# Kernel optimization log

Measured on AMD Instinct MI355X. Metric: run time of the kernel, lower is better.

The kernel has to match this reference:

```python
import jax, jax.numpy as jnp
import numpy as np

N, E, G = 50000, 800000, 128      # nodes, edges, graphs
IN, H, OUT = 128, 128, 2          # feature dims
K, L = 3, 3                       # Chebyshev order, num conv layers
EPS = 1e-5


def setup_inputs() -> dict:
    key = jax.random.key(0)
    ks = jax.random.split(key, 10)
    x = jax.random.normal(ks[0], (N, IN), dtype=jnp.float32)
    edge_index = jax.random.randint(ks[1], (2, E), 0, N, dtype=jnp.int64)
    batch = jnp.sort(jax.random.randint(ks[2], (N,), 0, G, dtype=jnp.int64))
    w_in = jax.random.normal(ks[3], (IN, H), dtype=jnp.float32) * 0.05
    b_in = jnp.zeros((H,), jnp.float32)
    ln_g = jnp.ones((H,), jnp.float32)
    ln_b = jnp.zeros((H,), jnp.float32)
    cheb_w = jax.random.normal(ks[4], (L, K, H, H), dtype=jnp.float32) * 0.05
    cheb_b = jnp.zeros((L, H), jnp.float32)
    bn_g = jnp.ones((L, H), jnp.float32)
    bn_b = jnp.zeros((L, H), jnp.float32)
    w1 = jax.random.normal(ks[5], (H, H // 2), dtype=jnp.float32) * 0.05
    b1 = jnp.zeros((H // 2,), jnp.float32)
    w2 = jax.random.normal(ks[6], (H // 2, OUT), dtype=jnp.float32) * 0.05
    b2 = jnp.zeros((OUT,), jnp.float32)
    return dict(x=x, w_in=w_in, b_in=b_in, ln_g=ln_g, ln_b=ln_b,
                cheb_w=cheb_w, cheb_b=cheb_b, bn_g=bn_g, bn_b=bn_b,
                w1=w1, b1=b1, w2=w2, b2=b2,
                edge_index=edge_index, batch=batch)


def reference(x, w_in, b_in, ln_g, ln_b, cheb_w, cheb_b, bn_g, bn_b,
              w1, b1, w2, b2, edge_index, batch):
    src, dst = edge_index[0], edge_index[1]

    # ChebConv scaled Laplacian with lambda_max=2, sym norm:
    # L_hat = -D^{-1/2} A D^{-1/2}  (self-loop terms cancel in PyG's __norm__)
    deg = jax.ops.segment_sum(jnp.ones((E,), x.dtype), src, num_segments=N)
    dinv = jnp.where(deg > 0, jax.lax.rsqrt(jnp.maximum(deg, 1.0)), 0.0)
    w_edge = -dinv[src] * dinv[dst]  # [E]

    def spmm(h):  # y_i = sum_{(j->i)} w_edge * h_j
        return jax.ops.segment_sum(w_edge[:, None] * h[src], dst, num_segments=N)

    # node_embed: Linear -> LayerNorm -> ReLU (dropout p used in eval => identity)
    h = x @ w_in + b_in
    mu = h.mean(-1, keepdims=True)
    var = h.var(-1, keepdims=True)
    h = (h - mu) * jax.lax.rsqrt(var + EPS) * ln_g + ln_b
    h = jax.nn.relu(h)

    hiddens = [h]
    for l in range(L):
        # Chebyshev recurrence: T0 = h, T1 = L_hat h, Tk = 2 L_hat T_{k-1} - T_{k-2}
        tx0 = h
        out = tx0 @ cheb_w[l, 0]
        tx1 = spmm(tx0)
        out = out + tx1 @ cheb_w[l, 1]
        for k in range(2, K):
            tx2 = 2.0 * spmm(tx1) - tx0
            out = out + tx2 @ cheb_w[l, k]
            tx0, tx1 = tx1, tx2
        out = out + cheb_b[l]
        # BatchNorm1d over nodes (training-mode batch statistics, biased var)
        m = out.mean(0)
        v = out.var(0)
        out = (out - m) * jax.lax.rsqrt(v + EPS) * bn_g[l] + bn_b[l]
        h = jax.nn.relu(out)
        hiddens.append(h)

    # Laplacian (Dirichlet) regularization over all hidden states
    reg = jnp.float32(0.0)
    for hh in hiddens:
        diff = hh[src] - hh[dst]              # [E, H]
        reg = reg + jnp.mean(jnp.sum(diff * diff, axis=-1))
    reg = reg / len(hiddens)

    # global mean pool over batch assignment
    counts = jax.ops.segment_sum(jnp.ones((N,), x.dtype), batch, num_segments=G)
    gsum = jax.ops.segment_sum(h, batch, num_segments=G)
    gmean = gsum / jnp.maximum(counts, 1.0)[:, None]

    z = jax.nn.relu(gmean @ w1 + b1)
    logits = z @ w2 + b2
    return logits, reg
```

## Files before the change

kernel.cpp:

```cpp
#include <hip/hip_runtime.h>
#include <hip/hip_bf16.h>

#define NNODES 50000
#define NEDGES 800000
#define NGRAPH 128
#define CAP 64
#define EPSV 1e-5f

typedef __attribute__((ext_vector_type(8))) short bf16x8;
typedef __attribute__((ext_vector_type(8))) unsigned short us16x8;
typedef __attribute__((ext_vector_type(4))) float f32x4;
typedef __attribute__((ext_vector_type(2))) float f32x2;

__device__ __forceinline__ unsigned short f2bf(float f) {
    unsigned u = __float_as_uint(f);
    return (unsigned short)((u + 0x7fffu + ((u >> 16) & 1u)) >> 16);
}
__device__ __forceinline__ float bf2f(unsigned short h) {
    return __uint_as_float(((unsigned)h) << 16);
}
__device__ __forceinline__ unsigned pk4_fp8(float a, float b, float c, float d) {
    int w = __builtin_amdgcn_cvt_pk_fp8_f32(a, b, 0, false);
    w = __builtin_amdgcn_cvt_pk_fp8_f32(c, d, w, true);
    return (unsigned)w;
}

__global__ void fillA_kernel(const int* __restrict__ src, const int* __restrict__ dst,
                             int* __restrict__ outdeg, int* __restrict__ indeg,
                             unsigned* __restrict__ slot, int E) {
    int e = blockIdx.x * blockDim.x + threadIdx.x;
    if (e < E) {
        int s = src[e];
        int d = dst[e];
        atomicAdd(&outdeg[s], 1);
        int pos = atomicAdd(&indeg[d], 1);
        if (pos < CAP) slot[(size_t)d * CAP + pos] = (unsigned)s;
    }
}

__global__ void pack_kernel(unsigned* __restrict__ slot, const int* __restrict__ indeg,
                            const int* __restrict__ outdeg,
                            const int* __restrict__ batch, int* __restrict__ gstart,
                            int total, int n) {
    if (blockIdx.x == 0 && threadIdx.x <= NGRAPH) {
        int g = threadIdx.x;
        int lo = 0, hi = n;
        while (lo < hi) {
            int mid = (lo + hi) >> 1;
            if (batch[mid] < g) lo = mid + 1; else hi = mid;
        }
        gstart[g] = lo;
    }
    int i = blockIdx.x * blockDim.x + threadIdx.x;
    if (i >= total) return;
    int node = i >> 6, k = i & (CAP - 1);
    int cnt = min(indeg[node], CAP);
    if (k < cnt) {
        unsigned idx = slot[i];
        int d = outdeg[idx];
        float dv = (d > 0) ? rsqrtf((float)d) : 0.0f;
        slot[i] = idx | ((unsigned)f2bf(dv) << 16);
    }
}

__global__ void wprep_kernel(const float* __restrict__ w_in, const float* __restrict__ cheb_w,
                             unsigned short* __restrict__ Wsp) {
    int p = blockIdx.x;
    int t = threadIdx.x;
    for (int s8 = 0; s8 < 8; ++s8) {
        int slot = s8 * 256 + t;
        int kc = slot >> 9, ct = (slot >> 6) & 7, lane = slot & 63;
        int q = lane >> 4, nn = lane & 15;
        unsigned short* o = Wsp + ((size_t)p * 2048 + slot) * 16;
#pragma unroll
        for (int j = 0; j < 8; ++j) {
            int k = kc * 32 + q * 8 + j, c = ct * 16 + nn;
            float v;
            if (p == 0) {
                v = w_in[k * 128 + c];
            } else {
                int pl = (p - 1) / 3, kk = (p - 1) % 3;
                v = cheb_w[((size_t)(pl * 3 + kk) * 128 + k) * 128 + c];
                if (kk == 0) v -= cheb_w[((size_t)(pl * 3 + 2) * 128 + k) * 128 + c];
                else if (kk == 2) v *= 2.f;
            }
            unsigned short hi = f2bf(v);
            o[j] = hi;
            o[8 + j] = f2bf(v - bf2f(hi));
        }
    }
}

template <int NPARTS, int EPI, int AF32>
__global__ __launch_bounds__(256) void gemm_mfma(
    const void* __restrict__ A0v, const void* __restrict__ A1v, const void* __restrict__ A2v,
    const unsigned short* __restrict__ Wsp, const float* __restrict__ bias,
    unsigned short* __restrict__ out16,
    const float* __restrict__ g0, const float* __restrict__ b0,
    float* __restrict__ colsum, float* __restrict__ colsumsq, int n) {
    __shared__ float red[256];
    int t = threadIdx.x, w = t >> 6, l = t & 63;
    int m = l & 15, qk = l >> 4;
    int rowA = blockIdx.x * 64 + w * 16 + m;
    red[t] = 0.f;
    __syncthreads();

    f32x4 acc[8];
#pragma unroll
    for (int ct = 0; ct < 8; ++ct) acc[ct] = (f32x4){0.f, 0.f, 0.f, 0.f};

    bool valid = rowA < n;
#pragma unroll
    for (int p = 0; p < NPARTS; ++p) {
#pragma unroll
        for (int kc = 0; kc < 4; ++kc) {
            bf16x8 ah, al;
            if (AF32) {
                const float* arow = (const float*)A0v;
                if (p == 1) arow = (const float*)A1v;
                if (p == 2) arow = (const float*)A2v;
                arow += (size_t)rowA * 128;
                float4 x0, x1;
                if (valid) {
                    x0 = *(const float4*)&arow[kc * 32 + qk * 8];
                    x1 = *(const float4*)&arow[kc * 32 + qk * 8 + 4];
                } else {
                    x0 = make_float4(0.f, 0.f, 0.f, 0.f); x1 = x0;
                }
                float xs[8] = {x0.x, x0.y, x0.z, x0.w, x1.x, x1.y, x1.z, x1.w};
#pragma unroll
                for (int j = 0; j < 8; ++j) {
                    unsigned short hi = f2bf(xs[j]);
                    ah[j] = (short)hi;
                    al[j] = (short)f2bf(xs[j] - bf2f(hi));
                }
            } else {
                const unsigned short* arow = (const unsigned short*)A0v;
                if (p == 1) arow = (const unsigned short*)A1v;
                if (p == 2) arow = (const unsigned short*)A2v;
                arow += (size_t)rowA * 128;
                if (valid) ah = *(const bf16x8*)&arow[kc * 32 + qk * 8];
                else ah = (bf16x8){0, 0, 0, 0, 0, 0, 0, 0};
            }
            const unsigned short* wb = Wsp + ((size_t)((p * 4 + kc) * 8) * 64 + l) * 16;
#pragma unroll
            for (int ct = 0; ct < 8; ++ct) {
                bf16x8 bh = *(const bf16x8*)(wb + (size_t)ct * 64 * 16);
                bf16x8 bl = *(const bf16x8*)(wb + (size_t)ct * 64 * 16 + 8);
                acc[ct] = __builtin_amdgcn_mfma_f32_16x16x32_bf16(ah, bh, acc[ct], 0, 0, 0);
                if (AF32)
                    acc[ct] = __builtin_amdgcn_mfma_f32_16x16x32_bf16(al, bh, acc[ct], 0, 0, 0);
                acc[ct] = __builtin_amdgcn_mfma_f32_16x16x32_bf16(ah, bl, acc[ct], 0, 0, 0);
            }
        }
    }

    int rowC0 = blockIdx.x * 64 + w * 16 + qk * 4;
    if (EPI == 0) {
        float rs[4] = {0.f, 0.f, 0.f, 0.f}, rss[4] = {0.f, 0.f, 0.f, 0.f};
#pragma unroll
        for (int ct = 0; ct < 8; ++ct) {
            float b = bias[ct * 16 + m];
#pragma unroll
            for (int j = 0; j < 4; ++j) {
                float v = acc[ct][j] + b;
                acc[ct][j] = v;
                rs[j] += v; rss[j] += v * v;
            }
        }
#pragma unroll
        for (int off = 1; off < 16; off <<= 1) {
#pragma unroll
            for (int j = 0; j < 4; ++j) {
                rs[j] += __shfl_xor(rs[j], off, 64);
                rss[j] += __shfl_xor(rss[j], off, 64);
            }
        }
        float mean[4], rstd[4];
#pragma unroll
        for (int j = 0; j < 4; ++j) {
            mean[j] = rs[j] * (1.f / 128.f);
            float var = rss[j] * (1.f / 128.f) - mean[j] * mean[j];
            rstd[j] = rsqrtf(var + EPSV);
        }
#pragma unroll
        for (int ct = 0; ct < 8; ++ct) {
            int c = ct * 16 + m;
            float gg = g0[c], bb = b0[c];
#pragma unroll
            for (int j = 0; j < 4; ++j) {
                int gr = rowC0 + j;
                if (gr < n) {
                    float x = (acc[ct][j] - mean[j]) * rstd[j] * gg + bb;
                    x = fmaxf(x, 0.f);
                    out16[(size_t)gr * 128 + c] = f2bf(x);
                }
            }
        }
    } else {
#pragma unroll
        for (int ct = 0; ct < 8; ++ct) {
            int c = ct * 16 + m;
            float b = bias[c];
            float s = 0.f, ss = 0.f;
#pragma unroll
            for (int j = 0; j < 4; ++j) {
                int gr = rowC0 + j;
                if (gr < n) {
                    float v = acc[ct][j] + b;
                    out16[(size_t)gr * 128 + c] = f2bf(v);
                    s += v; ss += v * v;
                }
            }
            s += __shfl_xor(s, 16, 64);  ss += __shfl_xor(ss, 16, 64);
            s += __shfl_xor(s, 32, 64);  ss += __shfl_xor(ss, 32, 64);
            if (qk == 0) {
                atomicAdd(&red[c], s);
                atomicAdd(&red[128 + c], ss);
            }
        }
        __syncthreads();
        if (t < 128) {
            atomicAdd(&colsum[t], red[t]);
            atomicAdd(&colsumsq[t], red[128 + t]);
        }
    }
}

__global__ void repack8_kernel(const unsigned short* __restrict__ h16,
                               unsigned char* __restrict__ h8, int total8) {
    int i = blockIdx.x * blockDim.x + threadIdx.x;
    if (i >= total8) return;
    us16x8 a = ((const us16x8*)h16)[i];
    uint2 o;
    o.x = pk4_fp8(bf2f(a[0]), bf2f(a[1]), bf2f(a[2]), bf2f(a[3]));
    o.y = pk4_fp8(bf2f(a[4]), bf2f(a[5]), bf2f(a[6]), bf2f(a[7]));
    ((uint2*)h8)[i] = o;
}

template <int MODE>
__global__ void spmm_g(const unsigned char* __restrict__ g8,
                       const unsigned short* __restrict__ self16,
                       unsigned short* __restrict__ dst16, unsigned char* __restrict__ dst8,
                       const unsigned* __restrict__ slot,
                       const int* __restrict__ outdeg, const int* __restrict__ indeg,
                       int n, double* __restrict__ norm_slots, double* __restrict__ cross_slots) {
    int lane = threadIdx.x & 63;
    int g = lane >> 4;
    int q = lane & 15;
    int w = (int)((blockIdx.x * (unsigned)blockDim.x + threadIdx.x) >> 6) * 4 + g;
    bool active = w < n;
    int cnt = active ? min(indeg[w], CAP) : 0;
    int od = active ? outdeg[w] : 0;
    float di = (od > 0) ? rsqrtf((float)od) : 0.f;
    size_t rbase = (size_t)w * 128 + q * 8;
    float hi[8];
    if (MODE != 1) {
#pragma unroll
        for (int j = 0; j < 8; ++j) hi[j] = 0.f;
        if (active) {
            us16x8 a = *(const us16x8*)&self16[rbase];
#pragma unroll
            for (int j = 0; j < 8; ++j) hi[j] = bf2f(a[j]);
        }
    }
    float acc[8];
#pragma unroll
    for (int j = 0; j < 8; ++j) acc[j] = 0.f;
    float cr = 0.f;
    size_t sbase = (size_t)w * CAP;
#pragma unroll
    for (int c = 0; c < 4; ++c) {
        if (c * 16 >= cnt) break;
        unsigned cw = (c * 16 + q < cnt) ? slot[sbase + c * 16 + q] : 0u;
        int mycnt = min(cnt - c * 16, 16);
        uint2 uu[16];
        float dd[16];
#pragma unroll
        for (int u = 0; u < 16; ++u) {
            unsigned cwu = __shfl(cw, (g << 4) + u, 64);
            int j = (int)(cwu & 0xFFFFu);
            dd[u] = bf2f((unsigned short)(cwu >> 16));
            uu[u] = make_uint2(0, 0);
            if (u < mycnt) uu[u] = *(const uint2*)&g8[(size_t)j * 128 + q * 8];
        }
#pragma unroll
        for (int u = 0; u < 16; ++u) {
            f32x2 l0 = __builtin_amdgcn_cvt_pk_f32_fp8(uu[u].x, false);
            f32x2 h0 = __builtin_amdgcn_cvt_pk_f32_fp8(uu[u].x, true);
            f32x2 l1 = __builtin_amdgcn_cvt_pk_f32_fp8(uu[u].y, false);
            f32x2 h1 = __builtin_amdgcn_cvt_pk_f32_fp8(uu[u].y, true);
            float v[8] = {l0.x, l0.y, h0.x, h0.y, l1.x, l1.y, h1.x, h1.y};
            if (MODE != 2) {
#pragma unroll
                for (int j = 0; j < 8; ++j) acc[j] += dd[u] * v[j];
            }
            if (MODE != 1) {
#pragma unroll
                for (int j = 0; j < 8; ++j) cr += hi[j] * v[j];
            }
        }
    }
    if (MODE != 2 && active) {
        float v[8];
        us16x8 o;
#pragma unroll
        for (int j = 0; j < 8; ++j) { v[j] = -di * acc[j]; o[j] = f2bf(v[j]); }
        *(us16x8*)&dst16[rbase] = o;
        if (MODE == 0) {
            uint2 o8;
            o8.x = pk4_fp8(v[0], v[1], v[2], v[3]);
            o8.y = pk4_fp8(v[4], v[5], v[6], v[7]);
            *(uint2*)&dst8[(size_t)w * 128 + q * 8] = o8;
        }
    }
    if (MODE != 1) {
        float nt = 0.f;
#pragma unroll
        for (int j = 0; j < 8; ++j) nt += hi[j] * hi[j];
#pragma unroll
        for (int off = 8; off > 0; off >>= 1) {
            cr += __shfl_down(cr, off, 16);
            nt += __shfl_down(nt, off, 16);
        }
        if (q == 0 && active) {
            int slotid = w & 255;
            atomicAdd(&cross_slots[slotid], (double)cr);
            atomicAdd(&norm_slots[slotid], (double)nt * (double)(od + indeg[w]));
        }
    }
}

__global__ void bnrelu_kernel(const unsigned short* __restrict__ ob16,
                              const float* __restrict__ colsum, const float* __restrict__ colsumsq,
                              const float* __restrict__ bn_g, const float* __restrict__ bn_b,
                              unsigned short* __restrict__ h16, unsigned char* __restrict__ h8,
                              int n, int total4) {
    __shared__ float ssc[128], ssh[128];
    int t = threadIdx.x;
    if (t < 128) {
        float m = colsum[t] / (float)n;
        float v = colsumsq[t] / (float)n - m * m;
        float sc = bn_g[t] * rsqrtf(v + EPSV);
        ssc[t] = sc;
        ssh[t] = bn_b[t] - m * sc;
    }
    __syncthreads();
    int i = blockIdx.x * blockDim.x + t;
    if (i >= total4) return;
    ushort4 o = ((const ushort4*)ob16)[i];
    int c = (i * 4) & 127;
    float4 r;
    r.x = fmaxf(bf2f(o.x) * ssc[c + 0] + ssh[c + 0], 0.f);
    r.y = fmaxf(bf2f(o.y) * ssc[c + 1] + ssh[c + 1], 0.f);
    r.z = fmaxf(bf2f(o.z) * ssc[c + 2] + ssh[c + 2], 0.f);
    r.w = fmaxf(bf2f(o.w) * ssc[c + 3] + ssh[c + 3], 0.f);
    ushort4 u = make_ushort4(f2bf(r.x), f2bf(r.y), f2bf(r.z), f2bf(r.w));
    ((ushort4*)h16)[i] = u;
    ((unsigned*)h8)[i] = pk4_fp8(r.x, r.y, r.z, r.w);
}

__global__ void poolmlp_kernel(const unsigned short* __restrict__ h16, const int* __restrict__ start,
                               const float* __restrict__ w1, const float* __restrict__ b1,
                               const float* __restrict__ w2, const float* __restrict__ b2,
                               const double* __restrict__ norm_slots,
                               const double* __restrict__ cross_slots,
                               float* __restrict__ out) {
    __shared__ float sm[2][128];
    __shared__ float gm[128];
    int g = blockIdx.x, t = threadIdx.x;
    int half = t >> 7, c = t & 127;
    int s = start[g], e = start[g + 1];
    float acc = 0.f;
    for (int r = s + half; r < e; r += 2) acc += bf2f(h16[(size_t)r * 128 + c]);
    sm[half][c] = acc;
    __syncthreads();
    if (t < 128) {
        float cnt = fmaxf((float)(e - s), 1.f);
        gm[t] = (sm[0][t] + sm[1][t]) / cnt;
    }
    __syncthreads();
    if (t < 64) {
        float z = b1[t];
        for (int k = 0; k < 128; ++k) z += gm[k] * w1[(size_t)k * 64 + t];
        z = fmaxf(z, 0.f);
        float p0 = z * w2[t * 2 + 0];
        float p1 = z * w2[t * 2 + 1];
        for (int off = 32; off > 0; off >>= 1) {
            p0 += __shfl_down(p0, off, 64);
            p1 += __shfl_down(p1, off, 64);
        }
        if (t == 0) {
            out[g * 2 + 0] = p0 + b2[0];
            out[g * 2 + 1] = p1 + b2[1];
        }
    } else if (g == 0 && t < 128) {
        int l = t - 64;
        double ns = 0.0, cs = 0.0;
        for (int i = l; i < 256; i += 64) { ns += norm_slots[i]; cs += cross_slots[i]; }
        for (int off = 32; off > 0; off >>= 1) {
            ns += __shfl_down(ns, off, 64);
            cs += __shfl_down(cs, off, 64);
        }
        if (l == 0) out[256] = (float)((ns - 2.0 * cs) / ((double)NEDGES * 4.0));
    }
}

extern "C" void kernel_launch(void* const* d_in, const int* in_sizes, int n_in,
                              void* d_out, int out_size, void* d_ws, size_t ws_size,
                              hipStream_t stream) {
    const float* x      = (const float*)d_in[0];
    const float* w_in   = (const float*)d_in[1];
    const float* b_in   = (const float*)d_in[2];
    const float* ln_g   = (const float*)d_in[3];
    const float* ln_b   = (const float*)d_in[4];
    const float* cheb_w = (const float*)d_in[5];
    const float* cheb_b = (const float*)d_in[6];
    const float* bn_g   = (const float*)d_in[7];
    const float* bn_b   = (const float*)d_in[8];
    const float* w1     = (const float*)d_in[9];
    const float* b1     = (const float*)d_in[10];
    const float* w2     = (const float*)d_in[11];
    const float* b2     = (const float*)d_in[12];
    const int*   eidx   = (const int*)d_in[13];
    const int*   batch  = (const int*)d_in[14];
    const int* src = eidx;
    const int* dst = eidx + NEDGES;
    float* out = (float*)d_out;

    char* ws = (char*)d_ws;
    size_t off = 0;
    auto alloc = [&](size_t bytes) -> void* {
        void* p = ws + off;
        off = (off + bytes + 255) & ~(size_t)255;
        return p;
    };
    unsigned short* ob16 = (unsigned short*)alloc((size_t)NNODES * 128 * 2);
    unsigned short* h16  = (unsigned short*)alloc((size_t)NNODES * 128 * 2);
    unsigned short* t116 = (unsigned short*)alloc((size_t)NNODES * 128 * 2);
    unsigned short* s16  = (unsigned short*)alloc((size_t)NNODES * 128 * 2);
    unsigned char*  h8   = (unsigned char*)alloc((size_t)NNODES * 128);
    unsigned char*  t18  = (unsigned char*)alloc((size_t)NNODES * 128);
    unsigned short* Wsp  = (unsigned short*)alloc((size_t)10 * 2048 * 16 * 2);
    int* degs     = (int*)alloc((size_t)2 * NNODES * 4);
    int* outdeg   = degs;
    int* indeg    = degs + NNODES;
    unsigned* slot = (unsigned*)alloc((size_t)NNODES * CAP * 4);
    int* gstart   = (int*)alloc((size_t)(NGRAPH + 1) * 4);
    float* colstats = (float*)alloc(768 * 4 + 512 * 8);
    double* dslots  = (double*)(colstats + 768);
    double* norm_slots  = dslots;
    double* cross_slots = dslots + 256;

    hipMemsetAsync(degs, 0, (size_t)2 * NNODES * 4, stream);
    hipMemsetAsync(colstats, 0, 768 * 4 + 512 * 8, stream);

    int tE = (NEDGES + 255) / 256;
    fillA_kernel<<<tE, 256, 0, stream>>>(src, dst, outdeg, indeg, slot, NEDGES);
    pack_kernel<<<(NNODES * CAP + 255) / 256, 256, 0, stream>>>(slot, indeg, outdeg,
                                                                batch, gstart,
                                                                NNODES * CAP, NNODES);
    wprep_kernel<<<10, 256, 0, stream>>>(w_in, cheb_w, Wsp);

    int gemmBlocks = (NNODES + 63) / 64;
    int nodes4 = (NNODES + 3) / 4;
    int spmmBlocks = (nodes4 * 64 + 255) / 256;
    int total4 = NNODES * 128 / 4;
    int total8 = NNODES * 128 / 8;

    gemm_mfma<1, 0, 1><<<gemmBlocks, 256, 0, stream>>>(x, nullptr, nullptr, Wsp, b_in, h16,
                                                       ln_g, ln_b, nullptr, nullptr, NNODES);
    repack8_kernel<<<(total8 + 255) / 256, 256, 0, stream>>>(h16, h8, total8);

    for (int l = 0; l < 3; ++l) {
        float* colsum = colstats + 256 * l;
        float* colsumsq = colsum + 128;
        spmm_g<0><<<spmmBlocks, 256, 0, stream>>>(h8, h16, t116, t18, slot,
                                                  outdeg, indeg, NNODES, norm_slots, cross_slots);
        spmm_g<1><<<spmmBlocks, 256, 0, stream>>>(t18, nullptr, s16, nullptr, slot,
                                                  outdeg, indeg, NNODES, nullptr, nullptr);
        gemm_mfma<3, 1, 0><<<gemmBlocks, 256, 0, stream>>>(h16, t116, s16,
            Wsp + (size_t)(1 + 3 * l) * 2048 * 16, cheb_b + (size_t)l * 128, ob16,
            nullptr, nullptr, colsum, colsumsq, NNODES);
        bnrelu_kernel<<<(total4 + 255) / 256, 256, 0, stream>>>(ob16, colsum, colsumsq,
            bn_g + (size_t)l * 128, bn_b + (size_t)l * 128, h16, h8, NNODES, total4);
    }
    spmm_g<2><<<spmmBlocks, 256, 0, stream>>>(h8, h16, nullptr, nullptr, slot,
                                              outdeg, indeg, NNODES, norm_slots, cross_slots);

    poolmlp_kernel<<<NGRAPH, 256, 0, stream>>>(h16, gstart, w1, b1, w2, b2,
                                               norm_slots, cross_slots, out);
}
```

Baseline: 684.1 us.

## Split fp8 feature tables into column halves for cache-resident SpMM gathers

Stores the fp8 node-feature copies as two 64-column half tables and runs each SpMM pass twice, once per half, with 8 lanes per node instead of 16. Each half table is about 3.2 MB, so the random neighbour gathers are meant to hit in L2/MALL instead of going to HBM. Streaming loads and stores of self rows, slot lists and outputs are marked nontemporal to avoid polluting the cache. The cost is twice as many launches and twice the slot-list and degree reads, and the regularization partial sums are now accumulated across two launches.

Result: slower. 865.6 us (+26.5%).

```diff
diff --git a/kernel.cpp b/kernel.cpp
--- a/kernel.cpp
+++ b/kernel.cpp
@@ -11,6 +11,7 @@
 typedef __attribute__((ext_vector_type(8))) unsigned short us16x8;
 typedef __attribute__((ext_vector_type(4))) float f32x4;
 typedef __attribute__((ext_vector_type(2))) float f32x2;
+typedef __attribute__((ext_vector_type(2))) unsigned u32x2;
 
 __device__ __forceinline__ unsigned short f2bf(float f) {
     unsigned u = __float_as_uint(f);
@@ -228,38 +229,44 @@
 }
 
 __global__ void repack8_kernel(const unsigned short* __restrict__ h16,
-                               unsigned char* __restrict__ h8, int total8) {
+                               unsigned char* __restrict__ h8a, unsigned char* __restrict__ h8b,
+                               int total8) {
     int i = blockIdx.x * blockDim.x + threadIdx.x;
     if (i >= total8) return;
     us16x8 a = ((const us16x8*)h16)[i];
-    uint2 o;
+    u32x2 o;
     o.x = pk4_fp8(bf2f(a[0]), bf2f(a[1]), bf2f(a[2]), bf2f(a[3]));
     o.y = pk4_fp8(bf2f(a[4]), bf2f(a[5]), bf2f(a[6]), bf2f(a[7]));
-    ((uint2*)h8)[i] = o;
+    int row = i >> 4;
+    int c = (i << 3) & 127;
+    unsigned char* dst = (c < 64) ? (h8a + (size_t)row * 64 + c)
+                                  : (h8b + (size_t)row * 64 + (c - 64));
+    __builtin_nontemporal_store(o, (u32x2*)dst);
 }
 
 template <int MODE>
-__global__ void spmm_g(const unsigned char* __restrict__ g8,
+__global__ void spmm_h(const unsigned char* __restrict__ g8h,
                        const unsigned short* __restrict__ self16,
-                       unsigned short* __restrict__ dst16, unsigned char* __restrict__ dst8,
+                       unsigned short* __restrict__ dst16, unsigned char* __restrict__ dst8h,
                        const unsigned* __restrict__ slot,
                        const int* __restrict__ outdeg, const int* __restrict__ indeg,
-                       int n, double* __restrict__ norm_slots, double* __restrict__ cross_slots) {
+                       int n, int colbase,
+                       double* __restrict__ norm_slots, double* __restrict__ cross_slots) {
     int lane = threadIdx.x & 63;
-    int g = lane >> 4;
-    int q = lane & 15;
-    int w = (int)((blockIdx.x * (unsigned)blockDim.x + threadIdx.x) >> 6) * 4 + g;
+    int g = lane >> 3;
+    int q = lane & 7;
+    int w = (int)((blockIdx.x * (unsigned)blockDim.x + threadIdx.x) >> 6) * 8 + g;
     bool active = w < n;
     int cnt = active ? min(indeg[w], CAP) : 0;
     int od = active ? outdeg[w] : 0;
     float di = (od > 0) ? rsqrtf((float)od) : 0.f;
-    size_t rbase = (size_t)w * 128 + q * 8;
     float hi[8];
     if (MODE != 1) {
 #pragma unroll
         for (int j = 0; j < 8; ++j) hi[j] = 0.f;
         if (active) {
-            us16x8 a = *(const us16x8*)&self16[rbase];
+            us16x8 a = __builtin_nontemporal_load(
+                (const us16x8*)&self16[(size_t)w * 128 + colbase + q * 8]);
 #pragma unroll
             for (int j = 0; j < 8; ++j) hi[j] = bf2f(a[j]);
         }
@@ -272,17 +279,27 @@
 #pragma unroll
     for (int c = 0; c < 4; ++c) {
         if (c * 16 >= cnt) break;
-        unsigned cw = (c * 16 + q < cnt) ? slot[sbase + c * 16 + q] : 0u;
+        unsigned s0 = 0, s1 = 0;
+        if (c * 16 + q < cnt)     s0 = __builtin_nontemporal_load(&slot[sbase + c * 16 + q]);
+        if (c * 16 + 8 + q < cnt) s1 = __builtin_nontemporal_load(&slot[sbase + c * 16 + 8 + q]);
         int mycnt = min(cnt - c * 16, 16);
-        uint2 uu[16];
+        u32x2 uu[16];
         float dd[16];
 #pragma unroll
-        for (int u = 0; u < 16; ++u) {
-            unsigned cwu = __shfl(cw, (g << 4) + u, 64);
-            int j = (int)(cwu & 0xFFFFu);
-            dd[u] = bf2f((unsigned short)(cwu >> 16));
-            uu[u] = make_uint2(0, 0);
-            if (u < mycnt) uu[u] = *(const uint2*)&g8[(size_t)j * 128 + q * 8];
+        for (int u = 0; u < 8; ++u) {
+            unsigned cw = (unsigned)__shfl((int)s0, (g << 3) + u, 64);
+            int j = (int)(cw & 0xFFFFu);
+            dd[u] = bf2f((unsigned short)(cw >> 16));
+            uu[u] = (u32x2){0, 0};
+            if (u < mycnt) uu[u] = *(const u32x2*)&g8h[(size_t)j * 64 + q * 8];
+        }
+#pragma unroll
+        for (int u = 0; u < 8; ++u) {
+            unsigned cw = (unsigned)__shfl((int)s1, (g << 3) + u, 64);
+            int j = (int)(cw & 0xFFFFu);
+            dd[8 + u] = bf2f((unsigned short)(cw >> 16));
+            uu[8 + u] = (u32x2){0, 0};
+            if (8 + u < mycnt) uu[8 + u] = *(const u32x2*)&g8h[(size_t)j * 64 + q * 8];
         }
 #pragma unroll
         for (int u = 0; u < 16; ++u) {
@@ -306,12 +323,12 @@
         us16x8 o;
 #pragma unroll
         for (int j = 0; j < 8; ++j) { v[j] = -di * acc[j]; o[j] = f2bf(v[j]); }
-        *(us16x8*)&dst16[rbase] = o;
+        __builtin_nontemporal_store(o, (us16x8*)&dst16[(size_t)w * 128 + colbase + q * 8]);
         if (MODE == 0) {
-            uint2 o8;
+            u32x2 o8;
             o8.x = pk4_fp8(v[0], v[1], v[2], v[3]);
             o8.y = pk4_fp8(v[4], v[5], v[6], v[7]);
-            *(uint2*)&dst8[(size_t)w * 128 + q * 8] = o8;
+            __builtin_nontemporal_store(o8, (u32x2*)&dst8h[(size_t)w * 64 + q * 8]);
         }
     }
     if (MODE != 1) {
@@ -319,9 +336,9 @@
 #pragma unroll
         for (int j = 0; j < 8; ++j) nt += hi[j] * hi[j];
 #pragma unroll
-        for (int off = 8; off > 0; off >>= 1) {
-            cr += __shfl_down(cr, off, 16);
-            nt += __shfl_down(nt, off, 16);
+        for (int off = 4; off > 0; off >>= 1) {
+            cr += __shfl_down(cr, off, 8);
+            nt += __shfl_down(nt, off, 8);
         }
         if (q == 0 && active) {
             int slotid = w & 255;
@@ -334,7 +351,8 @@
 __global__ void bnrelu_kernel(const unsigned short* __restrict__ ob16,
                               const float* __restrict__ colsum, const float* __restrict__ colsumsq,
                               const float* __restrict__ bn_g, const float* __restrict__ bn_b,
-                              unsigned short* __restrict__ h16, unsigned char* __restrict__ h8,
+                              unsigned short* __restrict__ h16,
+                              unsigned char* __restrict__ h8a, unsigned char* __restrict__ h8b,
                               int n, int total4) {
     __shared__ float ssc[128], ssh[128];
     int t = threadIdx.x;
@@ -357,7 +375,11 @@
     r.w = fmaxf(bf2f(o.w) * ssc[c + 3] + ssh[c + 3], 0.f);
     ushort4 u = make_ushort4(f2bf(r.x), f2bf(r.y), f2bf(r.z), f2bf(r.w));
     ((ushort4*)h16)[i] = u;
-    ((unsigned*)h8)[i] = pk4_fp8(r.x, r.y, r.z, r.w);
+    unsigned p8 = pk4_fp8(r.x, r.y, r.z, r.w);
+    int row = i >> 5;
+    unsigned char* dst = (c < 64) ? (h8a + (size_t)row * 64 + c)
+                                  : (h8b + (size_t)row * 64 + (c - 64));
+    __builtin_nontemporal_store(p8, (unsigned*)dst);
 }
 
 __global__ void poolmlp_kernel(const unsigned short* __restrict__ h16, const int* __restrict__ start,
@@ -439,8 +461,10 @@
     unsigned short* h16  = (unsigned short*)alloc((size_t)NNODES * 128 * 2);
     unsigned short* t116 = (unsigned short*)alloc((size_t)NNODES * 128 * 2);
     unsigned short* s16  = (unsigned short*)alloc((size_t)NNODES * 128 * 2);
-    unsigned char*  h8   = (unsigned char*)alloc((size_t)NNODES * 128);
-    unsigned char*  t18  = (unsigned char*)alloc((size_t)NNODES * 128);
+    unsigned char*  h8a  = (unsigned char*)alloc((size_t)NNODES * 64);
+    unsigned char*  h8b  = (unsigned char*)alloc((size_t)NNODES * 64);
+    unsigned char*  t18a = (unsigned char*)alloc((size_t)NNODES * 64);
+    unsigned char*  t18b = (unsigned char*)alloc((size_t)NNODES * 64);
     unsigned short* Wsp  = (unsigned short*)alloc((size_t)10 * 2048 * 16 * 2);
     int* degs     = (int*)alloc((size_t)2 * NNODES * 4);
     int* outdeg   = degs;
@@ -463,30 +487,36 @@
     wprep_kernel<<<10, 256, 0, stream>>>(w_in, cheb_w, Wsp);
 
     int gemmBlocks = (NNODES + 63) / 64;
-    int nodes4 = (NNODES + 3) / 4;
-    int spmmBlocks = (nodes4 * 64 + 255) / 256;
+    int nodes8 = (NNODES + 7) / 8;
+    int spmmBlocks = (nodes8 * 64 + 255) / 256;
     int total4 = NNODES * 128 / 4;
     int total8 = NNODES * 128 / 8;
 
     gemm_mfma<1, 0, 1><<<gemmBlocks, 256, 0, stream>>>(x, nullptr, nullptr, Wsp, b_in, h16,
                                                        ln_g, ln_b, nullptr, nullptr, NNODES);
-    repack8_kernel<<<(total8 + 255) / 256, 256, 0, stream>>>(h16, h8, total8);
+    repack8_kernel<<<(total8 + 255) / 256, 256, 0, stream>>>(h16, h8a, h8b, total8);
 
     for (int l = 0; l < 3; ++l) {
         float* colsum = colstats + 256 * l;
         float* colsumsq = colsum + 128;
-        spmm_g<0><<<spmmBlocks, 256, 0, stream>>>(h8, h16, t116, t18, slot,
-                                                  outdeg, indeg, NNODES, norm_slots, cross_slots);
-        spmm_g<1><<<spmmBlocks, 256, 0, stream>>>(t18, nullptr, s16, nullptr, slot,
-                                                  outdeg, indeg, NNODES, nullptr, nullptr);
+        spmm_h<0><<<spmmBlocks, 256, 0, stream>>>(h8a, h16, t116, t18a, slot,
+                                                  outdeg, indeg, NNODES, 0, norm_slots, cross_slots);
+        spmm_h<0><<<spmmBlocks, 256, 0, stream>>>(h8b, h16, t116, t18b, slot,
+                                                  outdeg, indeg, NNODES, 64, norm_slots, cross_slots);
+        spmm_h<1><<<spmmBlocks, 256, 0, stream>>>(t18a, nullptr, s16, nullptr, slot,
+                                                  outdeg, indeg, NNODES, 0, nullptr, nullptr);
+        spmm_h<1><<<spmmBlocks, 256, 0, stream>>>(t18b, nullptr, s16, nullptr, slot,
+                                                  outdeg, indeg, NNODES, 64, nullptr, nullptr);
         gemm_mfma<3, 1, 0><<<gemmBlocks, 256, 0, stream>>>(h16, t116, s16,
             Wsp + (size_t)(1 + 3 * l) * 2048 * 16, cheb_b + (size_t)l * 128, ob16,
             nullptr, nullptr, colsum, colsumsq, NNODES);
         bnrelu_kernel<<<(total4 + 255) / 256, 256, 0, stream>>>(ob16, colsum, colsumsq,
-            bn_g + (size_t)l * 128, bn_b + (size_t)l * 128, h16, h8, NNODES, total4);
-    }
-    spmm_g<2><<<spmmBlocks, 256, 0, stream>>>(h8, h16, nullptr, nullptr, slot,
-                                              outdeg, indeg, NNODES, norm_slots, cross_slots);
+            bn_g + (size_t)l * 128, bn_b + (size_t)l * 128, h16, h8a, h8b, NNODES, total4);
+    }
+    spmm_h<2><<<spmmBlocks, 256, 0, stream>>>(h8a, h16, nullptr, nullptr, slot,
+                                              outdeg, indeg, NNODES, 0, norm_slots, cross_slots);
+    spmm_h<2><<<spmmBlocks, 256, 0, stream>>>(h8b, h16, nullptr, nullptr, slot,
+                                              outdeg, indeg, NNODES, 64, norm_slots, cross_slots);
 
     poolmlp_kernel<<<NGRAPH, 256, 0, stream>>>(h16, gstart, w1, b1, w2, b2,
                                                norm_slots, cross_slots, out);
```
